# Optimization experiments

Hardware: AMD Instinct MI355X
Metric: run time of the kernel (lower is better)

The kernel has to match this reference:

```python
import jax, jax.numpy as jnp
import numpy as np

N_NODES = 131072
N_EDGES = 2097152
F_IN = 128
G_NODES = 256  # nodes per graph (equal-size graphs -> ptr = arange(0, N+1, 256))


def _linear(x, W, b):
    return x @ W + b


def _gin_conv(x, src, dst, W1, b1, W2, b2):
    # GINConv with eps=0: MLP(x + sum_{j->i} x_j)
    agg = jax.ops.segment_sum(x[src], dst, num_segments=x.shape[0])
    h = jax.nn.relu(_linear(x + agg, W1, b1))
    return _linear(h, W2, b2)


def _init(key, fan_in, fan_out):
    kw, kb = jax.random.split(key)
    s = 1.0 / np.sqrt(fan_in)
    W = jax.random.uniform(kw, (fan_in, fan_out), jnp.float32, -s, s)
    b = jax.random.uniform(kb, (fan_out,), jnp.float32, -s, s)
    return W, b


def setup_inputs() -> dict:
    key = jax.random.key(0)
    ks = jax.random.split(key, 14)
    x = jax.random.normal(ks[0], (N_NODES, F_IN), jnp.float32)
    edge_index = jax.random.randint(ks[1], (2, N_EDGES), 0, N_NODES, jnp.int64)
    W1a, b1a = _init(ks[2], F_IN, 128)
    W2a, b2a = _init(ks[3], 128, 128)
    W1b, b1b = _init(ks[4], 128, 128)
    W2b, b2b = _init(ks[5], 128, 128)
    Ws1, bs1 = _init(ks[6], 128, 32)
    Ws2, bs2 = _init(ks[7], 32, 32)
    Ws3, bs3 = _init(ks[8], 32, 32)
    Wm1, bm1 = _init(ks[9], 32 * 32, 32)
    Wm2, bm2 = _init(ks[10], 32, 32)
    Wm3, bm3 = _init(ks[11], 32, 2)
    return dict(x=x, edge_index=edge_index,
                W1a=W1a, b1a=b1a, W2a=W2a, b2a=b2a,
                W1b=W1b, b1b=b1b, W2b=W2b, b2b=b2b,
                Ws1=Ws1, bs1=bs1, Ws2=Ws2, bs2=bs2, Ws3=Ws3, bs3=bs3,
                Wm1=Wm1, bm1=bm1, Wm2=Wm2, bm2=bm2, Wm3=Wm3, bm3=bm3,
                nodes_per_graph=G_NODES)


def reference(x, edge_index, W1a, b1a, W2a, b2a, W1b, b1b, W2b, b2b,
              Ws1, bs1, Ws2, bs2, Ws3, bs3,
              Wm1, bm1, Wm2, bm2, Wm3, bm3, nodes_per_graph):
    src, dst = edge_index[0], edge_index[1]
    # two GINConv layers, each followed by outer ReLU (as in forward)
    h = jax.nn.relu(_gin_conv(x, src, dst, W1a, b1a, W2a, b2a))
    h = jax.nn.relu(_gin_conv(h, src, dst, W1b, b1b, W2b, b2b))
    # dropout is identity in eval mode; F.normalize(dim=1) row-wise L2
    hn = h / jnp.maximum(jnp.linalg.norm(h, axis=1, keepdims=True), 1e-12)
    s = jax.nn.relu(_linear(hn, Ws1, bs1))
    s = jax.nn.relu(_linear(s, Ws2, bs2))
    s = jax.nn.relu(_linear(s, Ws3, bs3))  # [N, 32]
    G = x.shape[0] // nodes_per_graph
    sg = s.reshape(G, nodes_per_graph, 32)
    # per-graph second-order pooling: graph.T @ graph, flattened
    HH = jnp.einsum('gnf,gne->gfe', sg, sg).reshape(G, 32 * 32)  # [G, 1024]
    o = jax.nn.relu(_linear(HH, Wm1, bm1))
    o = jax.nn.relu(_linear(o, Wm2, bm2))
    out = jax.nn.relu(_linear(o, Wm3, bm3))  # [G, 2]; output dropout identity in eval
    return (HH, out)
```

## Files before the change

kernel.cpp:

```cpp
#include <hip/hip_runtime.h>
#include <hip/hip_bf16.h>


#define NN 131072
#define NE 2097152
#define NG 512
#define NB 1024
#define ECAP 2560
#define CCAP 3328
#define ECH 8192

typedef unsigned short u16;
typedef unsigned int u32;
typedef __attribute__((ext_vector_type(8))) short short8;
typedef __attribute__((ext_vector_type(4))) float f32x4;

__device__ __forceinline__ float bf2f(u16 u) {
    union { u32 i; float f; } x; x.i = ((u32)u) << 16; return x.f;
}
__device__ __forceinline__ u16 f2bf(float f) {
    union { u32 i; float f; } x; x.f = f;
    u32 r = x.i + 0x7fffu + ((x.i >> 16) & 1u);
    return (u16)(r >> 16);
}

__global__ __launch_bounds__(256) void cast_x(const float* __restrict__ xf,
                                              u16* __restrict__ xb) {
    int i = blockIdx.x * 256 + threadIdx.x;
    const float4* src = (const float4*)xf;
    float4 a = src[2 * i], b = src[2 * i + 1];
    uint4 o;
    o.x = (u32)f2bf(a.x) | ((u32)f2bf(a.y) << 16);
    o.y = (u32)f2bf(a.z) | ((u32)f2bf(a.w) << 16);
    o.z = (u32)f2bf(b.x) | ((u32)f2bf(b.y) << 16);
    o.w = (u32)f2bf(b.z) | ((u32)f2bf(b.w) << 16);
    ((uint4*)xb)[i] = o;
}

__global__ __launch_bounds__(128) void zero_tail(u16* __restrict__ X0,
                                                 u16* __restrict__ H1) {
    int t = threadIdx.x;
    u32* a = (u32*)(X0 + (size_t)NN * 128);
    u32* b = (u32*)(H1 + (size_t)NN * 128);
    if (t < 64) a[t] = 0; else b[t - 64] = 0;
}

__global__ __launch_bounds__(256) void init_cursor(int* __restrict__ cursor) {
    int b = blockIdx.x * 256 + threadIdx.x;
    cursor[b] = b * ECAP;
}

__global__ __launch_bounds__(256) void bin_scatter(const int* __restrict__ gsrc,
                                                   const int* __restrict__ gdst,
                                                   int* __restrict__ cursor,
                                                   u32* __restrict__ ebuf) {
    __shared__ int lc[NB];
    __shared__ int rb[NB];
    __shared__ int lb[NB];
    int t = threadIdx.x;
    for (int i = 0; i < 4; ++i) lc[t + i * 256] = 0;
    __syncthreads();
    int base = blockIdx.x * ECH;
    for (int i = 0; i < ECH / 256; ++i) {
        int d = gdst[base + i * 256 + t];
        atomicAdd(&lc[d >> 7], 1);
    }
    __syncthreads();
    for (int i = 0; i < 4; ++i) {
        int b = t + i * 256;
        int c = lc[b];
        rb[b] = c ? atomicAdd(&cursor[b], c) : 0;
        lb[b] = 0;
    }
    __syncthreads();
    for (int i = 0; i < ECH / 256; ++i) {
        int idx = base + i * 256 + t;
        int d = gdst[idx];
        int s = gsrc[idx];
        int b = d >> 7;
        int o = atomicAdd(&lb[b], 1);
        ebuf[rb[b] + o] = ((u32)s << 7) | (u32)(d & 127);
    }
}

__global__ __launch_bounds__(512) void csr_sort(const u32* __restrict__ ebuf,
                                                const int* __restrict__ cursor,
                                                int* __restrict__ csr,
                                                int* __restrict__ start,
                                                int* __restrict__ deg,
                                                int* __restrict__ bcnt) {
    __shared__ int lcnt[128];
    __shared__ int lstart[128];
    __shared__ int lofs[128];
    int t = threadIdx.x, lane = t & 63, wave = t >> 6;
    int bkt = blockIdx.x;
    int e0 = bkt * ECAP;
    int n = cursor[bkt] - e0;
    if (t < 128) lcnt[t] = 0;
    __syncthreads();
    for (int j = t; j < n; j += 512)
        atomicAdd(&lcnt[ebuf[e0 + j] & 127], 1);
    __syncthreads();
    if (wave == 0) {
        int c0 = lcnt[2 * lane], c1 = lcnt[2 * lane + 1];
        int r0 = (c0 + 7) & ~7, r1 = (c1 + 7) & ~7;
        int s = r0 + r1, e = s;
        for (int o = 1; o < 64; o <<= 1) {
            int u = __shfl_up(e, o, 64);
            if (lane >= o) e += u;
        }
        int excl = e - s;
        lstart[2 * lane] = excl;          lofs[2 * lane] = excl;
        lstart[2 * lane + 1] = excl + r0; lofs[2 * lane + 1] = excl + r0;
        if (lane == 63) bcnt[bkt] = e;
    }
    __syncthreads();
    for (int j = t; j < n; j += 512) {
        u32 e = ebuf[e0 + j];
        int node = e & 127;
        int pos = atomicAdd(&lofs[node], 1);
        csr[bkt * CCAP + pos] = (int)(e >> 7);
    }
    __syncthreads();
    if (t < 128) {
        int c = lcnt[t];
        int cp = (c + 7) & ~7;
        int base = bkt * CCAP + lstart[t];
        for (int q = c; q < cp; ++q) csr[base + q] = NN;
        start[bkt * 128 + t] = base;
        deg[bkt * 128 + t] = cp;
    }
}

__global__ __launch_bounds__(256) void transpose_w(const float* a, const float* b,
                                                   const float* c, const float* d, u16* Wt) {
    const float* w = (blockIdx.x == 0) ? a : (blockIdx.x == 1) ? b : (blockIdx.x == 2) ? c : d;
    u16* o = Wt + blockIdx.x * 16384;
    for (int i = 0; i < 64; ++i) {
        int idx = threadIdx.x + i * 256;
        o[(idx & 127) * 128 + (idx >> 7)] = f2bf(w[idx]);
    }
}

__global__ __launch_bounds__(256) void transpose_small(const float* Ws1, const float* Ws2,
                                                       const float* Ws3, u16* Wsm) {
    int t = threadIdx.x;
    for (int i = 0; i < 16; ++i) {
        int idx = t + i * 256;
        int k = idx >> 5, n = idx & 31;
        Wsm[n * 128 + k] = f2bf(Ws1[idx]);
    }
    for (int i = 0; i < 4; ++i) {
        int idx = t + i * 256;
        int k = idx >> 5, n = idx & 31;
        Wsm[4096 + n * 32 + k] = f2bf(Ws2[idx]);
        Wsm[5120 + n * 32 + k] = f2bf(Ws3[idx]);
    }
}

__global__ __launch_bounds__(512, 8) void agg_mlp(const u16* __restrict__ X,
                                                  const int* __restrict__ csr,
                                                  const int* __restrict__ start,
                                                  const int* __restrict__ deg,
                                                  const int* __restrict__ bcnt,
                                                  const u16* __restrict__ Wt1,
                                                  const u16* __restrict__ Wt2,
                                                  const float* __restrict__ b1,
                                                  const float* __restrict__ b2,
                                                  u16* __restrict__ C) {
    __shared__ __align__(16) u16 As[128][136];
    __shared__ int sst[128];
    __shared__ int sdg[128];
    int tid = threadIdx.x, lane = tid & 63, wave = tid >> 6;
    int quad = lane >> 4, l16 = lane & 15;
    int bkt = blockIdx.x;
    size_t rowBase = (size_t)bkt * 128;
    const u32* Xu = (const u32*)X;
    int* Ls = (int*)&As[0][0];

    {
        int n4 = bcnt[bkt] >> 2;
        const int4* g4 = (const int4*)(csr + bkt * CCAP);
        int4* l4 = (int4*)Ls;
        for (int j = tid; j < n4; j += 512) l4[j] = g4[j];
        if (tid < 128) {
            sst[tid] = start[bkt * 128 + tid] - bkt * CCAP;
            sdg[tid] = deg[bkt * 128 + tid];
        }
    }
    __syncthreads();

    float a0[16], a1[16];
#pragma unroll
    for (int i = 0; i < 16; ++i) {
        int lrow = wave * 16 + i;
        int row = (int)rowBase + lrow;
        u32 v = Xu[(row << 6) + lane];
        a0[i] = bf2f((u16)v);
        a1[i] = bf2f((u16)(v >> 16));
        int st = sst[lrow];
        int de = sdg[lrow];
        for (int p = 0; p < de; p += 8) {
            int4 i0 = *(const int4*)&Ls[st + p];
            int4 i1 = *(const int4*)&Ls[st + p + 4];
            int s[8] = {i0.x, i0.y, i0.z, i0.w, i1.x, i1.y, i1.z, i1.w};
            u32 w[8];
#pragma unroll
            for (int k = 0; k < 8; ++k) w[k] = Xu[(s[k] << 6) + lane];
#pragma unroll
            for (int k = 0; k < 8; ++k) {
                a0[i] += bf2f((u16)w[k]);
                a1[i] += bf2f((u16)(w[k] >> 16));
            }
        }
    }
    __syncthreads();

#pragma unroll
    for (int i = 0; i < 16; ++i)
        *(u32*)&As[wave * 16 + i][2 * lane] =
            (u32)f2bf(a0[i]) | ((u32)f2bf(a1[i]) << 16);

    f32x4 acc[8];
#pragma unroll
    for (int t = 0; t < 8; ++t) acc[t] = (f32x4){0.f, 0.f, 0.f, 0.f};
#pragma unroll
    for (int c = 0; c < 4; ++c) {
        short8 a = *(const short8*)&As[wave * 16 + l16][c * 32 + quad * 8];
#pragma unroll
        for (int t = 0; t < 8; ++t) {
            short8 b = *(const short8*)(Wt1 + (t * 16 + l16) * 128 + c * 32 + quad * 8);
            acc[t] = __builtin_amdgcn_mfma_f32_16x16x32_bf16(a, b, acc[t], 0, 0, 0);
        }
    }
#pragma unroll
    for (int t = 0; t < 8; ++t) {
        int col = t * 16 + l16;
        float bv = b1[col];
#pragma unroll
        for (int r = 0; r < 4; ++r)
            As[wave * 16 + quad * 4 + r][col] = f2bf(fmaxf(acc[t][r] + bv, 0.f));
    }

    f32x4 acc2[8];
#pragma unroll
    for (int t = 0; t < 8; ++t) acc2[t] = (f32x4){0.f, 0.f, 0.f, 0.f};
#pragma unroll
    for (int c = 0; c < 4; ++c) {
        short8 a = *(const short8*)&As[wave * 16 + l16][c * 32 + quad * 8];
#pragma unroll
        for (int t = 0; t < 8; ++t) {
            short8 b = *(const short8*)(Wt2 + (t * 16 + l16) * 128 + c * 32 + quad * 8);
            acc2[t] = __builtin_amdgcn_mfma_f32_16x16x32_bf16(a, b, acc2[t], 0, 0, 0);
        }
    }
#pragma unroll
    for (int t = 0; t < 8; ++t) {
        int col = t * 16 + l16;
        float bv = b2[col];
#pragma unroll
        for (int r = 0; r < 4; ++r) {
            int row = wave * 16 + quad * 4 + r;
            C[(rowBase + row) * 128 + col] = f2bf(fmaxf(acc2[t][r] + bv, 0.f));
        }
    }
}

__global__ __launch_bounds__(256) void norm_mlp_mfma(const u16* __restrict__ X,
                                                     const u16* __restrict__ Wsm,
                                                     const float* __restrict__ bs1,
                                                     const float* __restrict__ bs2,
                                                     const float* __restrict__ bs3,
                                                     float* __restrict__ S) {
    __shared__ u16 As[64][136];
    __shared__ u16 W1s[32][136];
    __shared__ u16 W23s[2][32][40];
    __shared__ u16 H[64][40];
    int tid = threadIdx.x, lane = tid & 63, wave = tid >> 6;
    int quad = lane >> 4, l16 = lane & 15;
    size_t rowBase = (size_t)blockIdx.x * 64;

#pragma unroll
    for (int i = 0; i < 2; ++i) {
        int c = tid + i * 256;
        int r = c >> 4, co = (c & 15) << 3;
        *(uint4*)&W1s[r][co] = *(const uint4*)(Wsm + r * 128 + co);
    }
    {
        int which = tid >> 7, cc = tid & 127;
        int r = cc >> 2, co = (cc & 3) << 3;
        *(uint4*)&W23s[which][r][co] = *(const uint4*)(Wsm + 4096 + which * 1024 + r * 32 + co);
    }

    const u32* Xu = (const u32*)X;
    for (int i = 0; i < 16; ++i) {
        int row = wave * 16 + i;
        u32 v = Xu[(rowBase + row) * 64 + lane];
        float f0 = bf2f((u16)v), f1 = bf2f((u16)(v >> 16));
        float ss = f0 * f0 + f1 * f1;
        for (int o = 1; o < 64; o <<= 1) ss += __shfl_xor(ss, o, 64);
        float inv = 1.0f / fmaxf(sqrtf(ss), 1e-12f);
        *(u32*)&As[row][2 * lane] = (u32)f2bf(f0 * inv) | ((u32)f2bf(f1 * inv) << 16);
    }
    __syncthreads();

    f32x4 acc[2];
    acc[0] = (f32x4){0.f, 0.f, 0.f, 0.f};
    acc[1] = (f32x4){0.f, 0.f, 0.f, 0.f};
#pragma unroll
    for (int c = 0; c < 4; ++c) {
        short8 a = *(const short8*)&As[wave * 16 + l16][c * 32 + quad * 8];
#pragma unroll
        for (int t = 0; t < 2; ++t) {
            short8 b = *(const short8*)&W1s[t * 16 + l16][c * 32 + quad * 8];
            acc[t] = __builtin_amdgcn_mfma_f32_16x16x32_bf16(a, b, acc[t], 0, 0, 0);
        }
    }
#pragma unroll
    for (int t = 0; t < 2; ++t) {
        int col = t * 16 + l16;
        float bv = bs1[col];
#pragma unroll
        for (int r = 0; r < 4; ++r)
            H[wave * 16 + quad * 4 + r][col] = f2bf(fmaxf(acc[t][r] + bv, 0.f));
    }
    __syncthreads();

    f32x4 acc2[2];
    acc2[0] = (f32x4){0.f, 0.f, 0.f, 0.f};
    acc2[1] = (f32x4){0.f, 0.f, 0.f, 0.f};
    {
        short8 a = *(const short8*)&H[wave * 16 + l16][quad * 8];
#pragma unroll
        for (int t = 0; t < 2; ++t) {
            short8 b = *(const short8*)&W23s[0][t * 16 + l16][quad * 8];
            acc2[t] = __builtin_amdgcn_mfma_f32_16x16x32_bf16(a, b, acc2[t], 0, 0, 0);
        }
    }
    __syncthreads();
#pragma unroll
    for (int t = 0; t < 2; ++t) {
        int col = t * 16 + l16;
        float bv = bs2[col];
#pragma unroll
        for (int r = 0; r < 4; ++r)
            H[wave * 16 + quad * 4 + r][col] = f2bf(fmaxf(acc2[t][r] + bv, 0.f));
    }
    __syncthreads();

    f32x4 acc3[2];
    acc3[0] = (f32x4){0.f, 0.f, 0.f, 0.f};
    acc3[1] = (f32x4){0.f, 0.f, 0.f, 0.f};
    {
        short8 a = *(const short8*)&H[wave * 16 + l16][quad * 8];
#pragma unroll
        for (int t = 0; t < 2; ++t) {
            short8 b = *(const short8*)&W23s[1][t * 16 + l16][quad * 8];
            acc3[t] = __builtin_amdgcn_mfma_f32_16x16x32_bf16(a, b, acc3[t], 0, 0, 0);
        }
    }
#pragma unroll
    for (int t = 0; t < 2; ++t) {
        int col = t * 16 + l16;
        float bv = bs3[col];
#pragma unroll
        for (int r = 0; r < 4; ++r) {
            int row = wave * 16 + quad * 4 + r;
            S[(rowBase + row) * 32 + col] = fmaxf(acc3[t][r] + bv, 0.f);
        }
    }
}

__global__ __launch_bounds__(256) void gram(const float* __restrict__ S,
                                            float* __restrict__ out) {
    __shared__ float Sg[256 * 32];
    int t = threadIdx.x, g = blockIdx.x;
    const float4* src = (const float4*)(S + (size_t)g * 8192);
    float4* dst = (float4*)Sg;
    for (int i = 0; i < 8; ++i) dst[t + i * 256] = src[t + i * 256];
    __syncthreads();

    int f = t >> 3, e0 = (t & 7) << 2;
    float4 a = {0.f, 0.f, 0.f, 0.f};
    for (int n = 0; n < 256; ++n) {
        float sf = Sg[n * 32 + f];
        float4 se = *(const float4*)&Sg[n * 32 + e0];
        a.x += sf * se.x; a.y += sf * se.y; a.z += sf * se.z; a.w += sf * se.w;
    }
    *(float4*)(out + (size_t)g * 1024 + f * 32 + e0) = a;
}

__global__ __launch_bounds__(256) void graph_mlp(const float* __restrict__ HH,
                                                 const float* Wm1, const float* bm1,
                                                 const float* Wm2, const float* bm2,
                                                 const float* Wm3, const float* bm3,
                                                 float* __restrict__ out) {
    __shared__ float hh[1024];
    __shared__ float red[256];
    __shared__ float o1[32];
    __shared__ float o2[32];
    int t = threadIdx.x, g = blockIdx.x;
    ((float4*)hh)[t] = ((const float4*)(HH + (size_t)g * 1024))[t];
    __syncthreads();

    int j = t & 31, part = t >> 5;
    float p = 0.f;
    for (int i = 0; i < 128; ++i) { int k = part * 128 + i; p += hh[k] * Wm1[k * 32 + j]; }
    red[t] = p;
    __syncthreads();
    if (t < 32) {
        float s = 0.f;
        for (int q = 0; q < 8; ++q) s += red[q * 32 + t];
        o1[t] = fmaxf(s + bm1[t], 0.f);
    }
    __syncthreads();
    if (t < 32) {
        float s = 0.f;
        for (int k = 0; k < 32; ++k) s += o1[k] * Wm2[k * 32 + t];
        o2[t] = fmaxf(s + bm2[t], 0.f);
    }
    __syncthreads();
    if (t < 2) {
        float s = 0.f;
        for (int k = 0; k < 32; ++k) s += o2[k] * Wm3[k * 2 + t];
        out[524288 + g * 2 + t] = fmaxf(s + bm3[t], 0.f);
    }
}

extern "C" void kernel_launch(void* const* d_in, const int* in_sizes, int n_in,
                              void* d_out, int out_size, void* d_ws, size_t ws_size,
                              hipStream_t stream) {
    const float* x   = (const float*)d_in[0];
    const int*   ei  = (const int*)d_in[1];
    const float* W1a = (const float*)d_in[2];  const float* b1a = (const float*)d_in[3];
    const float* W2a = (const float*)d_in[4];  const float* b2a = (const float*)d_in[5];
    const float* W1b = (const float*)d_in[6];  const float* b1b = (const float*)d_in[7];
    const float* W2b = (const float*)d_in[8];  const float* b2b = (const float*)d_in[9];
    const float* Ws1 = (const float*)d_in[10]; const float* bs1 = (const float*)d_in[11];
    const float* Ws2 = (const float*)d_in[12]; const float* bs2 = (const float*)d_in[13];
    const float* Ws3 = (const float*)d_in[14]; const float* bs3 = (const float*)d_in[15];
    const float* Wm1 = (const float*)d_in[16]; const float* bm1 = (const float*)d_in[17];
    const float* Wm2 = (const float*)d_in[18]; const float* bm2 = (const float*)d_in[19];
    const float* Wm3 = (const float*)d_in[20]; const float* bm3 = (const float*)d_in[21];
    float* out = (float*)d_out;

    const int* gsrc = ei;
    const int* gdst = ei + NE;

    char* ws = (char*)d_ws;
    size_t off = 0;
    auto alloc = [&](size_t bytes) { size_t r = off; off = (off + bytes + 255) & ~(size_t)255; return r; };
    int*  cursor = (int*)(ws + alloc((size_t)NB * 4));
    int*  bcnt   = (int*)(ws + alloc((size_t)NB * 4));
    u32*  ebuf   = (u32*)(ws + alloc((size_t)NB * ECAP * 4));
    int*  csr    = (int*)(ws + alloc((size_t)NB * CCAP * 4));
    int*  stA    = (int*)(ws + alloc((size_t)NN * 4));
    int*  dgA    = (int*)(ws + alloc((size_t)NN * 4));
    u16*  Wt     = (u16*)(ws + alloc(4 * 16384 * 2));
    u16*  Wsm    = (u16*)(ws + alloc(6144 * 2));
    u16*  X0     = (u16*)(ws + alloc((size_t)(NN + 1) * 128 * 2));
    u16*  H1     = (u16*)(ws + alloc((size_t)(NN + 1) * 128 * 2));
    float* S     = (float*)ebuf;
    (void)ws_size; (void)n_in; (void)in_sizes; (void)out_size;

    init_cursor<<<NB / 256, 256, 0, stream>>>(cursor);
    bin_scatter<<<NE / ECH, 256, 0, stream>>>(gsrc, gdst, cursor, ebuf);
    csr_sort<<<NB, 512, 0, stream>>>(ebuf, cursor, csr, stA, dgA, bcnt);

    cast_x<<<NN * 128 / (256 * 8), 256, 0, stream>>>(x, X0);
    zero_tail<<<1, 128, 0, stream>>>(X0, H1);
    transpose_w<<<4, 256, 0, stream>>>(W1a, W2a, W1b, W2b, Wt);
    transpose_small<<<1, 256, 0, stream>>>(Ws1, Ws2, Ws3, Wsm);

    agg_mlp<<<NN / 128, 512, 0, stream>>>(X0, csr, stA, dgA, bcnt,
                                          Wt + 0 * 16384, Wt + 1 * 16384, b1a, b2a, H1);
    agg_mlp<<<NN / 128, 512, 0, stream>>>(H1, csr, stA, dgA, bcnt,
                                          Wt + 2 * 16384, Wt + 3 * 16384, b1b, b2b, X0);

    norm_mlp_mfma<<<NN / 64, 256, 0, stream>>>(X0, Wsm, bs1, bs2, bs3, S);
    gram<<<NG, 256, 0, stream>>>(S, out);
    graph_mlp<<<NG, 256, 0, stream>>>(out, Wm1, bm1, Wm2, bm2, Wm3, bm3, out);
}
```

Before: 588.4 us.

## Split fused aggregation+MLP into separate gather kernel and LDS-staged GEMM kernel

Unfuses the GIN layer into an aggregation kernel that writes the aggregated rows to a temporary bf16 buffer, followed by a separate two-layer MLP kernel. The MLP kernel stages both weight matrices in shared memory instead of reading them from global memory per MFMA. The aim is to relieve register pressure and raise occupancy in the latency-bound gather, and to cut redundant weight loads in the GEMM. In exchange it adds an extra round trip of the activation tensor through global memory and two extra launches.

```diff
diff --git a/kernel.cpp b/kernel.cpp
--- a/kernel.cpp
+++ b/kernel.cpp
@@ -158,25 +158,20 @@
     }
 }
 
-__global__ __launch_bounds__(512, 8) void agg_mlp(const u16* __restrict__ X,
-                                                  const int* __restrict__ csr,
-                                                  const int* __restrict__ start,
-                                                  const int* __restrict__ deg,
-                                                  const int* __restrict__ bcnt,
-                                                  const u16* __restrict__ Wt1,
-                                                  const u16* __restrict__ Wt2,
-                                                  const float* __restrict__ b1,
-                                                  const float* __restrict__ b2,
-                                                  u16* __restrict__ C) {
-    __shared__ __align__(16) u16 As[128][136];
+__global__ __launch_bounds__(512) void aggregate_csr(const u16* __restrict__ X,
+                                                     const int* __restrict__ csr,
+                                                     const int* __restrict__ start,
+                                                     const int* __restrict__ deg,
+                                                     const int* __restrict__ bcnt,
+                                                     u16* __restrict__ T) {
+    __shared__ __align__(16) int Ls[CCAP];
     __shared__ int sst[128];
     __shared__ int sdg[128];
     int tid = threadIdx.x, lane = tid & 63, wave = tid >> 6;
-    int quad = lane >> 4, l16 = lane & 15;
     int bkt = blockIdx.x;
-    size_t rowBase = (size_t)bkt * 128;
+    int rowBase = bkt * 128;
     const u32* Xu = (const u32*)X;
-    int* Ls = (int*)&As[0][0];
+    u32* Tu = (u32*)T;
 
     {
         int n4 = bcnt[bkt] >> 2;
@@ -190,14 +185,11 @@
     }
     __syncthreads();
 
-    float a0[16], a1[16];
-#pragma unroll
     for (int i = 0; i < 16; ++i) {
         int lrow = wave * 16 + i;
-        int row = (int)rowBase + lrow;
-        u32 v = Xu[(row << 6) + lane];
-        a0[i] = bf2f((u16)v);
-        a1[i] = bf2f((u16)(v >> 16));
+        int row = rowBase + lrow;
+        u32 v = Xu[((size_t)row << 6) + lane];
+        float a0 = bf2f((u16)v), a1 = bf2f((u16)(v >> 16));
         int st = sst[lrow];
         int de = sdg[lrow];
         for (int p = 0; p < de; p += 8) {
@@ -206,20 +198,48 @@
             int s[8] = {i0.x, i0.y, i0.z, i0.w, i1.x, i1.y, i1.z, i1.w};
             u32 w[8];
 #pragma unroll
-            for (int k = 0; k < 8; ++k) w[k] = Xu[(s[k] << 6) + lane];
+            for (int k = 0; k < 8; ++k) w[k] = Xu[((size_t)s[k] << 6) + lane];
 #pragma unroll
             for (int k = 0; k < 8; ++k) {
-                a0[i] += bf2f((u16)w[k]);
-                a1[i] += bf2f((u16)(w[k] >> 16));
+                a0 += bf2f((u16)w[k]);
+                a1 += bf2f((u16)(w[k] >> 16));
             }
         }
-    }
-    __syncthreads();
-
-#pragma unroll
-    for (int i = 0; i < 16; ++i)
-        *(u32*)&As[wave * 16 + i][2 * lane] =
-            (u32)f2bf(a0[i]) | ((u32)f2bf(a1[i]) << 16);
+        Tu[((size_t)row << 6) + lane] = (u32)f2bf(a0) | ((u32)f2bf(a1) << 16);
+    }
+}
+
+__global__ __launch_bounds__(256) void gemm2_relu(const u16* __restrict__ A,
+                                                  const u16* __restrict__ Wt1,
+                                                  const u16* __restrict__ Wt2,
+                                                  const float* __restrict__ b1,
+                                                  const float* __restrict__ b2,
+                                                  u16* __restrict__ C) {
+    __shared__ u16 As[64][136];
+    __shared__ u16 Ws[128][136];
+    int tid = threadIdx.x;
+    size_t rowBase = (size_t)blockIdx.x * 64;
+
+    uint4 w2r[8];
+#pragma unroll
+    for (int i = 0; i < 8; ++i) {
+        int c = tid + i * 256;
+        w2r[i] = *(const uint4*)(Wt2 + (c >> 4) * 128 + ((c & 15) << 3));
+    }
+    for (int i = 0; i < 4; ++i) {
+        int c = tid + i * 256;
+        int r = c >> 4, co = (c & 15) << 3;
+        *(uint4*)&As[r][co] = *(const uint4*)(A + (rowBase + r) * 128 + co);
+    }
+    for (int i = 0; i < 8; ++i) {
+        int c = tid + i * 256;
+        int r = c >> 4, co = (c & 15) << 3;
+        *(uint4*)&Ws[r][co] = *(const uint4*)(Wt1 + r * 128 + co);
+    }
+    __syncthreads();
+
+    int lane = tid & 63, wave = tid >> 6;
+    int quad = lane >> 4, l16 = lane & 15;
 
     f32x4 acc[8];
 #pragma unroll
@@ -229,10 +249,11 @@
         short8 a = *(const short8*)&As[wave * 16 + l16][c * 32 + quad * 8];
 #pragma unroll
         for (int t = 0; t < 8; ++t) {
-            short8 b = *(const short8*)(Wt1 + (t * 16 + l16) * 128 + c * 32 + quad * 8);
+            short8 b = *(const short8*)&Ws[t * 16 + l16][c * 32 + quad * 8];
             acc[t] = __builtin_amdgcn_mfma_f32_16x16x32_bf16(a, b, acc[t], 0, 0, 0);
         }
     }
+
 #pragma unroll
     for (int t = 0; t < 8; ++t) {
         int col = t * 16 + l16;
@@ -241,6 +262,14 @@
         for (int r = 0; r < 4; ++r)
             As[wave * 16 + quad * 4 + r][col] = f2bf(fmaxf(acc[t][r] + bv, 0.f));
     }
+    __syncthreads();
+
+#pragma unroll
+    for (int i = 0; i < 8; ++i) {
+        int c = tid + i * 256;
+        *(uint4*)&Ws[c >> 4][(c & 15) << 3] = w2r[i];
+    }
+    __syncthreads();
 
     f32x4 acc2[8];
 #pragma unroll
@@ -250,7 +279,7 @@
         short8 a = *(const short8*)&As[wave * 16 + l16][c * 32 + quad * 8];
 #pragma unroll
         for (int t = 0; t < 8; ++t) {
-            short8 b = *(const short8*)(Wt2 + (t * 16 + l16) * 128 + c * 32 + quad * 8);
+            short8 b = *(const short8*)&Ws[t * 16 + l16][c * 32 + quad * 8];
             acc2[t] = __builtin_amdgcn_mfma_f32_16x16x32_bf16(a, b, acc2[t], 0, 0, 0);
         }
     }
@@ -460,6 +489,7 @@
     u16*  Wsm    = (u16*)(ws + alloc(6144 * 2));
     u16*  X0     = (u16*)(ws + alloc((size_t)(NN + 1) * 128 * 2));
     u16*  H1     = (u16*)(ws + alloc((size_t)(NN + 1) * 128 * 2));
+    u16*  T      = (u16*)(ws + alloc((size_t)NN * 128 * 2));
     float* S     = (float*)ebuf;
     (void)ws_size; (void)n_in; (void)in_sizes; (void)out_size;
 
@@ -472,10 +502,10 @@
     transpose_w<<<4, 256, 0, stream>>>(W1a, W2a, W1b, W2b, Wt);
     transpose_small<<<1, 256, 0, stream>>>(Ws1, Ws2, Ws3, Wsm);
 
-    agg_mlp<<<NN / 128, 512, 0, stream>>>(X0, csr, stA, dgA, bcnt,
-                                          Wt + 0 * 16384, Wt + 1 * 16384, b1a, b2a, H1);
-    agg_mlp<<<NN / 128, 512, 0, stream>>>(H1, csr, stA, dgA, bcnt,
-                                          Wt + 2 * 16384, Wt + 3 * 16384, b1b, b2b, X0);
+    aggregate_csr<<<NB, 512, 0, stream>>>(X0, csr, stA, dgA, bcnt, T);
+    gemm2_relu<<<NN / 64, 256, 0, stream>>>(T, Wt + 0 * 16384, Wt + 1 * 16384, b1a, b2a, H1);
+    aggregate_csr<<<NB, 512, 0, stream>>>(H1, csr, stA, dgA, bcnt, T);
+    gemm2_relu<<<NN / 64, 256, 0, stream>>>(T, Wt + 2 * 16384, Wt + 3 * 16384, b1b, b2b, X0);
 
     norm_mlp_mfma<<<NN / 64, 256, 0, stream>>>(X0, Wsm, bs1, bs2, bs3, S);
     gram<<<NG, 256, 0, stream>>>(S, out);
```

New measurement: 512.4 us. -12.9%, faster.
